# Optimization experiments

Measured on AMD Instinct MI355X. Metric: run time of the kernel, lower is better.

Reference implementation:

```python
import jax, jax.numpy as jnp
import numpy as np
import math

B, S, IN_DIM = 2048, 60, 211
D, H, L, DFF, NC = 192, 6, 3, 768, 35
DK = D // H


def make_pe(seq_len, d_model):
    pos = np.arange(seq_len)[:, None].astype(np.float32)
    div = np.exp(np.arange(0, d_model, 2).astype(np.float32) * (-math.log(10000.0) / d_model))
    pe = np.zeros((seq_len, d_model), dtype=np.float32)
    pe[:, 0::2] = np.sin(pos * div)
    pe[:, 1::2] = np.cos(pos * div)
    return jnp.asarray(pe)


def setup_inputs() -> dict:
    key = jax.random.key(0)
    ks = jax.random.split(key, 24)
    r = lambda k, shape, fan: jax.random.normal(k, shape, jnp.float32) * (1.0 / np.sqrt(fan))
    inp = {
        'x': jax.random.normal(ks[0], (B, S, IN_DIM), jnp.float32),
        'W_in': r(ks[1], (IN_DIM, D), IN_DIM), 'b_in': jnp.zeros((D,), jnp.float32),
        'pe': make_pe(S, D),
        'Wq': r(ks[2], (L, D, D), D), 'bq': jnp.zeros((L, D), jnp.float32),
        'Wk': r(ks[3], (L, D, D), D), 'bk': jnp.zeros((L, D), jnp.float32),
        'Wv': r(ks[4], (L, D, D), D), 'bv': jnp.zeros((L, D), jnp.float32),
        'Wo': r(ks[5], (L, D, D), D), 'bo': jnp.zeros((L, D), jnp.float32),
        'W1': r(ks[6], (L, D, DFF), D), 'b1': jnp.zeros((L, DFF), jnp.float32),
        'W2': r(ks[7], (L, DFF, D), DFF), 'b2': jnp.zeros((L, D), jnp.float32),
        'g1': jnp.ones((L, D), jnp.float32), 'be1': jnp.zeros((L, D), jnp.float32),
        'g2': jnp.ones((L, D), jnp.float32), 'be2': jnp.zeros((L, D), jnp.float32),
        'Wc1': r(ks[8], (D, D // 2), D), 'bc1': jnp.zeros((D // 2,), jnp.float32),
        'Wc2': r(ks[9], (D // 2, NC), D // 2), 'bc2': jnp.zeros((NC,), jnp.float32),
    }
    return inp


def layer_norm(x, g, b, eps=1e-5):
    mu = jnp.mean(x, axis=-1, keepdims=True)
    var = jnp.mean((x - mu) ** 2, axis=-1, keepdims=True)
    return (x - mu) * jax.lax.rsqrt(var + eps) * g + b


def mha(x, Wq, bq, Wk, bk, Wv, bv, Wo, bo):
    Bs, Ss, _ = x.shape
    q = (x @ Wq + bq).reshape(Bs, Ss, H, DK)
    k = (x @ Wk + bk).reshape(Bs, Ss, H, DK)
    v = (x @ Wv + bv).reshape(Bs, Ss, H, DK)
    scores = jnp.einsum('bqhd,bkhd->bhqk', q, k) / jnp.sqrt(jnp.float32(DK))
    attn = jax.nn.softmax(scores, axis=-1)
    ctx = jnp.einsum('bhqk,bkhd->bqhd', attn, v).reshape(Bs, Ss, D)
    return ctx @ Wo + bo


def encoder_layer(x, Wq, bq, Wk, bk, Wv, bv, Wo, bo, W1, b1, W2, b2, g1, be1, g2, be2):
    attn_out = mha(x, Wq, bq, Wk, bk, Wv, bv, Wo, bo)
    x = layer_norm(x + attn_out, g1, be1)
    ff = jax.nn.gelu(x @ W1 + b1, approximate=False) @ W2 + b2
    return layer_norm(x + ff, g2, be2)


def reference(x, W_in, b_in, pe, Wq, bq, Wk, bk, Wv, bv, Wo, bo,
              W1, b1, W2, b2, g1, be1, g2, be2, Wc1, bc1, Wc2, bc2):
    h = x @ W_in + b_in + pe  # [B,S,D]
    for l in range(L):
        h = encoder_layer(h, Wq[l], bq[l], Wk[l], bk[l], Wv[l], bv[l], Wo[l], bo[l],
                          W1[l], b1[l], W2[l], b2[l], g1[l], be1[l], g2[l], be2[l])
    hidden = jax.nn.gelu(h @ Wc1 + bc1, approximate=False)
    return hidden @ Wc2 + bc2  # [B,S,NC]
```

## Files before the change

### kernel.cpp

```cpp
#include <hip/hip_runtime.h>
#include <cmath>

#define B_   2048
#define S_   60
#define NTOK (B_*S_)
#define IND_ 211
#define D_   192
#define H_   6
#define DK_  32
#define L_   3
#define DFF_ 768
#define NC_  35
#define DH_  96

typedef unsigned short us_t;
typedef us_t us8 __attribute__((ext_vector_type(8)));
typedef us_t us4 __attribute__((ext_vector_type(4)));
typedef short sh8 __attribute__((ext_vector_type(8)));
typedef float f4 __attribute__((ext_vector_type(4)));

#define MFMA(a, b, cc) __builtin_amdgcn_mfma_f32_16x16x32_bf16((a), (b), (cc), 0, 0, 0)
#define ZACC(A, M, N) \
    for (int _i = 0; _i < (M); ++_i) \
        for (int _j = 0; _j < (N); ++_j) { \
            A[_i][_j][0] = 0.f; A[_i][_j][1] = 0.f; A[_i][_j][2] = 0.f; A[_i][_j][3] = 0.f; }
#define ZACC1(A, N) \
    for (int _j = 0; _j < (N); ++_j) { \
        A[_j][0] = 0.f; A[_j][1] = 0.f; A[_j][2] = 0.f; A[_j][3] = 0.f; }

__device__ __forceinline__ float bf2f(us_t u) {
    union { unsigned int i; float f; } v; v.i = ((unsigned int)u) << 16; return v.f;
}
__device__ __forceinline__ us_t f2bf(float f) {
    union { float f; unsigned int i; } v; v.f = f;
    unsigned int r = v.i + 0x7fffu + ((v.i >> 16) & 1u);
    return (us_t)(r >> 16);
}
__device__ __forceinline__ float gelu_f(float v) {
    float u = v * (0.7978845608f + 0.0356774081f * v * v);
    float e = __expf(2.f * u);
    float t = 1.f - 2.f / (e + 1.f);
    return 0.5f * v * (1.f + t);
}
__device__ __forceinline__ void gld16(const us_t* g, us_t* s) {
    __builtin_amdgcn_global_load_lds(
        (const __attribute__((address_space(1))) unsigned int*)(g),
        (__attribute__((address_space(3))) unsigned int*)(s), 16, 0, 0);
}

__global__ void prep_t(const float* __restrict__ in, us_t* __restrict__ out,
                       int K, int Kpad, int N)
{
    int e = blockIdx.x * 256 + threadIdx.x;
    if (e >= N * Kpad) return;
    int n = e / Kpad, kp = e % Kpad;
    out[e] = (kp < K) ? f2bf(in[(size_t)kp * N + n]) : (us_t)0;
}

__global__ void prep_ff(const float* __restrict__ W1, const float* __restrict__ W2,
                        us_t* __restrict__ W1T, us_t* __restrict__ W2T)
{
    int e = blockIdx.x * 256 + threadIdx.x;
    if (e >= L_ * 12 * 13824) return;
    int l = e / (12 * 13824), r = e % (12 * 13824);
    int tile = r / 13824, q = r % 13824;
    int col = q / 72, kk = q % 72;
    int cb = tile / 3, pc = tile % 3;
    us_t v1 = 0, v2 = 0;
    if (kk < 64) {
        v1 = f2bf(W1[((size_t)l * D_ + pc * 64 + kk) * DFF_ + cb * D_ + col]);
        v2 = f2bf(W2[((size_t)l * DFF_ + cb * D_ + pc * 64 + kk) * D_ + col]);
    }
    W1T[e] = v1; W2T[e] = v2;
}

__global__ __launch_bounds__(256) void inp_mfma(
    const float* __restrict__ x, const us_t* __restrict__ Wint,
    const float* __restrict__ b_in, const float* __restrict__ pe,
    us_t* __restrict__ h)
{
    __shared__ __align__(16) char smem[29696 + 27648];
    us_t* Xs = (us_t*)smem;
    us_t* Ws = (us_t*)(smem + 29696);
    const int tid = threadIdx.x;
    const int lane = tid & 63, wid = tid >> 6;
    const int g = lane >> 4, c = lane & 15;
    const int wr = wid >> 1, wc = wid & 1;
    const int row0 = blockIdx.x * 64;

    for (int e = tid; e < 64 * 224; e += 256) {
        int tok = e / 224, kp = e % 224;
        float v = (kp < IND_) ? x[(size_t)(row0 + tok) * IND_ + kp] : 0.f;
        Xs[tok * 232 + kp] = f2bf(v);
    }

    f4 acc[2][6];
    ZACC(acc, 2, 6);
    for (int pc = 0; pc < 4; ++pc) {
        __syncthreads();
        const int nk = (pc < 3) ? 64 : 32;
        const int per = nk / 8;
        for (int e = tid; e < 192 * per; e += 256) {
            int rw = e / per, v = e % per;
            *(us8*)&Ws[rw * 72 + v * 8] =
                *(const us8*)&Wint[(size_t)rw * 224 + pc * 64 + v * 8];
        }
        __syncthreads();
        for (int kk = 0; kk < nk / 32; ++kk) {
            const int ka = pc * 64 + kk * 32 + g * 8;
            const int kw = kk * 32 + g * 8;
            sh8 a0 = *(const sh8*)&Xs[(32 * wr + c) * 232 + ka];
            sh8 a1 = *(const sh8*)&Xs[(32 * wr + 16 + c) * 232 + ka];
            #pragma unroll
            for (int ni = 0; ni < 6; ++ni) {
                sh8 bf = *(const sh8*)&Ws[(96 * wc + 16 * ni + c) * 72 + kw];
                acc[0][ni] = MFMA(a0, bf, acc[0][ni]);
                acc[1][ni] = MFMA(a1, bf, acc[1][ni]);
            }
        }
    }
    #pragma unroll
    for (int ni = 0; ni < 6; ++ni) {
        const int col = 96 * wc + 16 * ni + c;
        const float bv = b_in[col];
        #pragma unroll
        for (int mi = 0; mi < 2; ++mi)
            #pragma unroll
            for (int r = 0; r < 4; ++r) {
                int tokg = row0 + 32 * wr + 16 * mi + 4 * g + r;
                int s = tokg % S_;
                float val = acc[mi][ni][r] + bv + pe[(size_t)s * D_ + col];
                h[(size_t)tokg * D_ + col] = f2bf(val);
            }
    }
}

__global__ __launch_bounds__(512) void qkv_attn_wo(
    us_t* __restrict__ h,
    const us_t* __restrict__ Wqt, const us_t* __restrict__ Wkt,
    const us_t* __restrict__ Wvt, const us_t* __restrict__ Wot,
    const float* __restrict__ bq, const float* __restrict__ bk,
    const float* __restrict__ bv, const float* __restrict__ bo,
    const float* __restrict__ g1, const float* __restrict__ be1)
{
    __shared__ __align__(16) char smem[157696];
    us_t* Xs = (us_t*)smem;
    us_t* Qs = (us_t*)(smem + 25600);
    us_t* Ks = (us_t*)(smem + 51200);
    us_t* Vt = (us_t*)(smem + 76800);
    us_t* Ws = (us_t*)(smem + 104448);
    us_t* P0 = (us_t*)(smem + 104448);
    us_t* P1 = (us_t*)(smem + 113664);
    us_t* Cx = (us_t*)(smem + 132096);
    float* eL = (float*)(smem + 51200);

    const int tid = threadIdx.x;
    const int lane = tid & 63, wid = tid >> 6;
    const int g = lane >> 4, c = lane & 15;
    const int wr = wid >> 2, wc = wid & 3;
    us_t* hb = h + (size_t)blockIdx.x * (S_ * D_);

    for (int e = tid; e < 1536; e += 512) {
        int tok = e / 24, v = e % 24;
        us8 u = {0, 0, 0, 0, 0, 0, 0, 0};
        if (tok < S_) u = *(const us8*)&hb[(size_t)tok * D_ + v * 8];
        *(us8*)&Xs[tok * 200 + v * 8] = u;
    }

    for (int m = 0; m < 3; ++m) {
        const us_t* Wt = (m == 0) ? Wqt : (m == 1) ? Wkt : Wvt;
        const float* bb = (m == 0) ? bq : (m == 1) ? bk : bv;
        f4 acc[2][3];
        ZACC(acc, 2, 3);
        for (int pc = 0; pc < 3; ++pc) {
            __syncthreads();
            for (int e = tid; e < 1536; e += 512) {
                int rw = e >> 3, v = e & 7;
                *(us8*)&Ws[rw * 72 + v * 8] =
                    *(const us8*)&Wt[(size_t)rw * 192 + pc * 64 + v * 8];
            }
            __syncthreads();
            #pragma unroll
            for (int kk = 0; kk < 2; ++kk) {
                const int ka = pc * 64 + kk * 32 + g * 8;
                const int kw = kk * 32 + g * 8;
                sh8 a0 = *(const sh8*)&Xs[(32 * wr + c) * 200 + ka];
                sh8 a1 = *(const sh8*)&Xs[(32 * wr + 16 + c) * 200 + ka];
                #pragma unroll
                for (int ni = 0; ni < 3; ++ni) {
                    sh8 bf = *(const sh8*)&Ws[(48 * wc + 16 * ni + c) * 72 + kw];
                    acc[0][ni] = MFMA(a0, bf, acc[0][ni]);
                    acc[1][ni] = MFMA(a1, bf, acc[1][ni]);
                }
            }
        }
        #pragma unroll
        for (int ni = 0; ni < 3; ++ni) {
            const int col = 48 * wc + 16 * ni + c;
            const float bval = bb[col];
            #pragma unroll
            for (int mi = 0; mi < 2; ++mi)
                #pragma unroll
                for (int r = 0; r < 4; ++r) {
                    int tok = 32 * wr + 16 * mi + 4 * g + r;
                    us_t o = f2bf(acc[mi][ni][r] + bval);
                    if (m == 0)      Qs[tok * 200 + col] = o;
                    else if (m == 1) Ks[tok * 200 + col] = o;
                    else             Vt[col * 72 + tok] = o;
                }
        }
    }
    __syncthreads();

    const int hgrp = wid & 3;
    const int hsel = wid >> 2;
    for (int rr = 0; rr < 3; ++rr) {
        const int hh = 2 * rr + hsel;
        us_t* Pb = hsel ? P1 : P0;
        f4 sc[4];
        ZACC1(sc, 4);
        {
            const int ka = 32 * hh + g * 8;
            sh8 aq = *(const sh8*)&Qs[(16 * hgrp + c) * 200 + ka];
            #pragma unroll
            for (int ni = 0; ni < 4; ++ni) {
                sh8 bk8 = *(const sh8*)&Ks[(16 * ni + c) * 200 + ka];
                sc[ni] = MFMA(aq, bk8, sc[ni]);
            }
        }
        #pragma unroll
        for (int r = 0; r < 4; ++r) {
            float mx = -1e30f;
            #pragma unroll
            for (int ni = 0; ni < 4; ++ni) {
                float v = sc[ni][r] * 0.17677669529663687f;
                if (16 * ni + c >= S_) v = -1e30f;
                sc[ni][r] = v;
                mx = fmaxf(mx, v);
            }
            mx = fmaxf(mx, __shfl_xor(mx, 1));
            mx = fmaxf(mx, __shfl_xor(mx, 2));
            mx = fmaxf(mx, __shfl_xor(mx, 4));
            mx = fmaxf(mx, __shfl_xor(mx, 8));
            float sum = 0.f;
            #pragma unroll
            for (int ni = 0; ni < 4; ++ni) {
                float e = __expf(sc[ni][r] - mx);
                sc[ni][r] = e; sum += e;
            }
            sum += __shfl_xor(sum, 1);
            sum += __shfl_xor(sum, 2);
            sum += __shfl_xor(sum, 4);
            sum += __shfl_xor(sum, 8);
            const float inv = 1.f / sum;
            #pragma unroll
            for (int ni = 0; ni < 4; ++ni)
                Pb[(16 * hgrp + 4 * g + r) * 72 + 16 * ni + c] = f2bf(sc[ni][r] * inv);
        }
        __syncthreads();
        f4 ov[2];
        ZACC1(ov, 2);
        #pragma unroll
        for (int kk = 0; kk < 2; ++kk) {
            sh8 ap = *(const sh8*)&Pb[(16 * hgrp + c) * 72 + kk * 32 + g * 8];
            #pragma unroll
            for (int n2 = 0; n2 < 2; ++n2) {
                sh8 bv8 = *(const sh8*)&Vt[(32 * hh + 16 * n2 + c) * 72 + kk * 32 + g * 8];
                ov[n2] = MFMA(ap, bv8, ov[n2]);
            }
        }
        #pragma unroll
        for (int n2 = 0; n2 < 2; ++n2)
            #pragma unroll
            for (int r = 0; r < 4; ++r)
                Cx[(16 * hgrp + 4 * g + r) * 200 + 32 * hh + 16 * n2 + c] = f2bf(ov[n2][r]);
        __syncthreads();
    }

    f4 aw[2][3];
    ZACC(aw, 2, 3);
    for (int pc = 0; pc < 3; ++pc) {
        __syncthreads();
        for (int e = tid; e < 1536; e += 512) {
            int rw = e >> 3, v = e & 7;
            *(us8*)&Ws[rw * 72 + v * 8] =
                *(const us8*)&Wot[(size_t)rw * 192 + pc * 64 + v * 8];
        }
        __syncthreads();
        #pragma unroll
        for (int kk = 0; kk < 2; ++kk) {
            const int ka = pc * 64 + kk * 32 + g * 8;
            const int kw = kk * 32 + g * 8;
            sh8 a0 = *(const sh8*)&Cx[(32 * wr + c) * 200 + ka];
            sh8 a1 = *(const sh8*)&Cx[(32 * wr + 16 + c) * 200 + ka];
            #pragma unroll
            for (int ni = 0; ni < 3; ++ni) {
                sh8 bf = *(const sh8*)&Ws[(48 * wc + 16 * ni + c) * 72 + kw];
                aw[0][ni] = MFMA(a0, bf, aw[0][ni]);
                aw[1][ni] = MFMA(a1, bf, aw[1][ni]);
            }
        }
    }
    __syncthreads();
    #pragma unroll
    for (int ni = 0; ni < 3; ++ni) {
        const int col = 48 * wc + 16 * ni + c;
        const float bov = bo[col];
        #pragma unroll
        for (int mi = 0; mi < 2; ++mi)
            #pragma unroll
            for (int r = 0; r < 4; ++r) {
                int tok = 32 * wr + 16 * mi + 4 * g + r;
                eL[tok * 200 + col] = aw[mi][ni][r] + bov + bf2f(Xs[tok * 200 + col]);
            }
    }
    __syncthreads();
    {
        const int tok = tid >> 3, t8 = tid & 7;
        float vals[24], sum = 0.f, ssq = 0.f;
        #pragma unroll
        for (int jv = 0; jv < 6; ++jv) {
            float4 v4 = *(const float4*)&eL[tok * 200 + t8 * 24 + jv * 4];
            vals[jv*4+0] = v4.x; vals[jv*4+1] = v4.y; vals[jv*4+2] = v4.z; vals[jv*4+3] = v4.w;
            sum += v4.x + v4.y + v4.z + v4.w;
            ssq += v4.x*v4.x + v4.y*v4.y + v4.z*v4.z + v4.w*v4.w;
        }
        sum += __shfl_xor(sum, 1); sum += __shfl_xor(sum, 2); sum += __shfl_xor(sum, 4);
        ssq += __shfl_xor(ssq, 1); ssq += __shfl_xor(ssq, 2); ssq += __shfl_xor(ssq, 4);
        const float mean = sum * (1.f / D_);
        const float var  = ssq * (1.f / D_) - mean * mean;
        const float rstd = rsqrtf(var + 1e-5f);
        if (tok < S_) {
            #pragma unroll
            for (int jv = 0; jv < 6; ++jv) {
                us4 o4;
                #pragma unroll
                for (int j = 0; j < 4; ++j) {
                    int col = t8 * 24 + jv * 4 + j;
                    o4[j] = f2bf((vals[jv*4+j] - mean) * rstd * g1[col] + be1[col]);
                }
                *(us4*)&hb[(size_t)tok * D_ + t8 * 24 + jv * 4] = o4;
            }
        }
    }
}

__device__ __forceinline__ void ff_tile(const us_t* A, f4 (&acc)[2][6],
                                        const us_t* W, int pc,
                                        int wr, int wc, int g, int c)
{
    #pragma unroll
    for (int kk = 0; kk < 2; ++kk) {
        const int ka = pc * 64 + kk * 32 + g * 8;
        const int kw = kk * 32 + g * 8;
        sh8 a0 = *(const sh8*)&A[(32 * wr + c) * 200 + ka];
        sh8 a1 = *(const sh8*)&A[(32 * wr + 16 + c) * 200 + ka];
        #pragma unroll
        for (int ni = 0; ni < 6; ++ni) {
            sh8 bf = *(const sh8*)&W[(96 * wc + 16 * ni + c) * 72 + kw];
            acc[0][ni] = MFMA(a0, bf, acc[0][ni]);
            acc[1][ni] = MFMA(a1, bf, acc[1][ni]);
        }
    }
}

__global__ __launch_bounds__(512) void ff_mfma(
    us_t* __restrict__ hio,
    const us_t* __restrict__ W1T, const float* __restrict__ b1,
    const us_t* __restrict__ W2T, const float* __restrict__ b2,
    const float* __restrict__ gamma, const float* __restrict__ beta)
{
    __shared__ __align__(16) char smem[157696];
    us_t* Xs  = (us_t*)smem;
    us_t* Ts  = (us_t*)(smem + 51200);
    us_t* Wsb = (us_t*)(smem + 102400);
    float* eL = (float*)(smem + 51200);

    const int tid = threadIdx.x;
    const int lane = tid & 63, wid = tid >> 6;
    const int g = lane >> 4, c = lane & 15;
    const int wr = wid >> 1, wc = wid & 1;
    const int row0 = blockIdx.x * 128;

    auto stageW = [&](int t) {
        const int cb2 = t / 6, ph = (t % 6) / 3, pc2 = t % 3;
        const us_t* src = (ph ? W2T : W1T) + (size_t)(cb2 * 3 + pc2) * 13824;
        us_t* dst = Wsb + (size_t)(t & 1) * 13824;
        #pragma unroll
        for (int i = wid; i < 27; i += 8)
            gld16(src + i * 512 + lane * 8, dst + i * 512);
    };

    for (int e = tid; e < 3072; e += 512) {
        int tok = e / 24, v = e % 24;
        *(us8*)&Xs[tok * 200 + v * 8] = *(const us8*)&hio[(size_t)(row0 + tok) * D_ + v * 8];
    }
    stageW(0);
    __syncthreads();

    f4 acc2[2][6];
    ZACC(acc2, 2, 6);
    for (int cb = 0; cb < 4; ++cb) {
        f4 acc1[2][6];
        ZACC(acc1, 2, 6);
        #pragma unroll
        for (int pc = 0; pc < 3; ++pc) {
            const int t = cb * 6 + pc;
            if (t < 23) stageW(t + 1);
            ff_tile(Xs, acc1, Wsb + (size_t)(t & 1) * 13824, pc, wr, wc, g, c);
            if (pc == 2) {
                #pragma unroll
                for (int ni = 0; ni < 6; ++ni) {
                    const int col = 96 * wc + 16 * ni + c;
                    const float b1v = b1[cb * 192 + col];
                    #pragma unroll
                    for (int mi = 0; mi < 2; ++mi)
                        #pragma unroll
                        for (int r = 0; r < 4; ++r) {
                            int tok = 32 * wr + 16 * mi + 4 * g + r;
                            Ts[tok * 200 + col] = f2bf(gelu_f(acc1[mi][ni][r] + b1v));
                        }
                }
            }
            __syncthreads();
        }
        #pragma unroll
        for (int pc = 0; pc < 3; ++pc) {
            const int t = cb * 6 + 3 + pc;
            if (t < 23) stageW(t + 1);
            ff_tile(Ts, acc2, Wsb + (size_t)(t & 1) * 13824, pc, wr, wc, g, c);
            __syncthreads();
        }
    }

    for (int p = 0; p < 2; ++p) {
        if (p) __syncthreads();
        if ((wr >> 1) == p) {
            #pragma unroll
            for (int ni = 0; ni < 6; ++ni) {
                const int col = 96 * wc + 16 * ni + c;
                const float b2v = b2[col];
                #pragma unroll
                for (int mi = 0; mi < 2; ++mi)
                    #pragma unroll
                    for (int r = 0; r < 4; ++r) {
                        int tok = 32 * wr + 16 * mi + 4 * g + r;
                        eL[(tok - 64 * p) * 200 + col] =
                            acc2[mi][ni][r] + b2v + bf2f(Xs[tok * 200 + col]);
                    }
            }
        }
        __syncthreads();
        {
            const int tl = tid >> 3, t8 = tid & 7;
            float vals[24], sum = 0.f, ssq = 0.f;
            #pragma unroll
            for (int jv = 0; jv < 6; ++jv) {
                float4 v4 = *(const float4*)&eL[tl * 200 + t8 * 24 + jv * 4];
                vals[jv*4+0] = v4.x; vals[jv*4+1] = v4.y;
                vals[jv*4+2] = v4.z; vals[jv*4+3] = v4.w;
                sum += v4.x + v4.y + v4.z + v4.w;
                ssq += v4.x*v4.x + v4.y*v4.y + v4.z*v4.z + v4.w*v4.w;
            }
            sum += __shfl_xor(sum, 1); sum += __shfl_xor(sum, 2); sum += __shfl_xor(sum, 4);
            ssq += __shfl_xor(ssq, 1); ssq += __shfl_xor(ssq, 2); ssq += __shfl_xor(ssq, 4);
            const float mean = sum * (1.f / D_);
            const float var  = ssq * (1.f / D_) - mean * mean;
            const float rstd = rsqrtf(var + 1e-5f);
            #pragma unroll
            for (int jv = 0; jv < 6; ++jv) {
                us4 o4;
                #pragma unroll
                for (int j = 0; j < 4; ++j) {
                    int col = t8 * 24 + jv * 4 + j;
                    o4[j] = f2bf((vals[jv*4+j] - mean) * rstd * gamma[col] + beta[col]);
                }
                *(us4*)&hio[(size_t)(row0 + 64 * p + tl) * D_ + t8 * 24 + jv * 4] = o4;
            }
        }
    }
}

__global__ __launch_bounds__(256) void clf1_mfma(
    const us_t* __restrict__ h, const us_t* __restrict__ Wc1t,
    const float* __restrict__ bc1, us_t* __restrict__ hid)
{
    __shared__ __align__(16) char smem[25600 + 13824];
    us_t* Xs = (us_t*)smem;
    us_t* Ws = (us_t*)(smem + 25600);
    const int tid = threadIdx.x;
    const int lane = tid & 63, wid = tid >> 6;
    const int g = lane >> 4, c = lane & 15;
    const int wr = wid >> 1, wc = wid & 1;
    const int row0 = blockIdx.x * 64;

    for (int e = tid; e < 1536; e += 256) {
        int tok = e / 24, v = e % 24;
        *(us8*)&Xs[tok * 200 + v * 8] = *(const us8*)&h[(size_t)(row0 + tok) * D_ + v * 8];
    }
    f4 acc[2][3];
    ZACC(acc, 2, 3);
    for (int pc = 0; pc < 3; ++pc) {
        __syncthreads();
        for (int e = tid; e < 768; e += 256) {
            int rw = e >> 3, v = e & 7;
            *(us8*)&Ws[rw * 72 + v * 8] =
                *(const us8*)&Wc1t[(size_t)rw * 192 + pc * 64 + v * 8];
        }
        __syncthreads();
        #pragma unroll
        for (int kk = 0; kk < 2; ++kk) {
            const int ka = pc * 64 + kk * 32 + g * 8;
            const int kw = kk * 32 + g * 8;
            sh8 a0 = *(const sh8*)&Xs[(32 * wr + c) * 200 + ka];
            sh8 a1 = *(const sh8*)&Xs[(32 * wr + 16 + c) * 200 + ka];
            #pragma unroll
            for (int ni = 0; ni < 3; ++ni) {
                sh8 bf = *(const sh8*)&Ws[(48 * wc + 16 * ni + c) * 72 + kw];
                acc[0][ni] = MFMA(a0, bf, acc[0][ni]);
                acc[1][ni] = MFMA(a1, bf, acc[1][ni]);
            }
        }
    }
    #pragma unroll
    for (int ni = 0; ni < 3; ++ni) {
        const int col = 48 * wc + 16 * ni + c;
        const float bv = bc1[col];
        #pragma unroll
        for (int mi = 0; mi < 2; ++mi)
            #pragma unroll
            for (int r = 0; r < 4; ++r) {
                int tok = row0 + 32 * wr + 16 * mi + 4 * g + r;
                hid[(size_t)tok * DH_ + col] = f2bf(gelu_f(acc[mi][ni][r] + bv));
            }
    }
}

__global__ __launch_bounds__(256) void clf2_kernel(
    const us_t* __restrict__ hid, const float* __restrict__ Wc2,
    const float* __restrict__ bc2, float* __restrict__ out)
{
    __shared__ us_t Hs[64 * 104];
    __shared__ float Wl[DH_ * NC_];
    __shared__ float bl[NC_];
    const int tid = threadIdx.x;
    const int row0 = blockIdx.x * 64;
    for (int e = tid; e < 768; e += 256) {
        int tok = e / 12, v = e % 12;
        *(us8*)&Hs[tok * 104 + v * 8] = *(const us8*)&hid[(size_t)(row0 + tok) * DH_ + v * 8];
    }
    for (int e = tid; e < DH_ * NC_; e += 256) Wl[e] = Wc2[e];
    if (tid < NC_) bl[tid] = bc2[tid];
    __syncthreads();
    for (int e = tid; e < 64 * NC_; e += 256) {
        const int tok = e / NC_, col = e % NC_;
        float acc = bl[col];
        #pragma unroll 8
        for (int kk = 0; kk < DH_; ++kk)
            acc = fmaf(bf2f(Hs[tok * 104 + kk]), Wl[kk * NC_ + col], acc);
        out[(size_t)(row0 + tok) * NC_ + col] = acc;
    }
}

extern "C" void kernel_launch(void* const* d_in, const int* in_sizes, int n_in,
                              void* d_out, int out_size, void* d_ws, size_t ws_size,
                              hipStream_t stream)
{
    const float* x    = (const float*)d_in[0];
    const float* W_in = (const float*)d_in[1];
    const float* b_in = (const float*)d_in[2];
    const float* pe   = (const float*)d_in[3];
    const float* Wq   = (const float*)d_in[4];
    const float* bq   = (const float*)d_in[5];
    const float* Wk   = (const float*)d_in[6];
    const float* bk   = (const float*)d_in[7];
    const float* Wv   = (const float*)d_in[8];
    const float* bv   = (const float*)d_in[9];
    const float* Wo   = (const float*)d_in[10];
    const float* bo   = (const float*)d_in[11];
    const float* W1   = (const float*)d_in[12];
    const float* b1   = (const float*)d_in[13];
    const float* W2   = (const float*)d_in[14];
    const float* b2   = (const float*)d_in[15];
    const float* g1   = (const float*)d_in[16];
    const float* be1  = (const float*)d_in[17];
    const float* g2   = (const float*)d_in[18];
    const float* be2  = (const float*)d_in[19];
    const float* Wc1  = (const float*)d_in[20];
    const float* bc1  = (const float*)d_in[21];
    const float* Wc2  = (const float*)d_in[22];
    const float* bc2  = (const float*)d_in[23];
    float* outp = (float*)d_out;

    us_t* h    = (us_t*)d_ws;
    us_t* hid  = h + (size_t)NTOK * D_;
    us_t* Wint = hid + (size_t)NTOK * DH_;
    us_t* Wqt  = Wint + 192 * 224;
    us_t* Wkt  = Wqt + 3 * 36864;
    us_t* Wvt  = Wkt + 3 * 36864;
    us_t* Wot  = Wvt + 3 * 36864;
    us_t* W1T  = Wot + 3 * 36864;
    us_t* W2T  = W1T + (size_t)L_ * 12 * 13824;
    us_t* Wc1t = W2T + (size_t)L_ * 12 * 13824;

    prep_t<<<168, 256, 0, stream>>>(W_in, Wint, IND_, 224, D_);
    for (int l = 0; l < L_; ++l) {
        prep_t<<<144, 256, 0, stream>>>(Wq + (size_t)l * 36864, Wqt + (size_t)l * 36864, 192, 192, 192);
        prep_t<<<144, 256, 0, stream>>>(Wk + (size_t)l * 36864, Wkt + (size_t)l * 36864, 192, 192, 192);
        prep_t<<<144, 256, 0, stream>>>(Wv + (size_t)l * 36864, Wvt + (size_t)l * 36864, 192, 192, 192);
        prep_t<<<144, 256, 0, stream>>>(Wo + (size_t)l * 36864, Wot + (size_t)l * 36864, 192, 192, 192);
    }
    prep_ff<<<(L_ * 12 * 13824 + 255) / 256, 256, 0, stream>>>(W1, W2, W1T, W2T);
    prep_t<<<72, 256, 0, stream>>>(Wc1, Wc1t, 192, 192, DH_);

    inp_mfma<<<NTOK / 64, 256, 0, stream>>>(x, Wint, b_in, pe, h);

    for (int l = 0; l < L_; ++l) {
        qkv_attn_wo<<<B_, 512, 0, stream>>>(
            h,
            Wqt + (size_t)l * 36864, Wkt + (size_t)l * 36864,
            Wvt + (size_t)l * 36864, Wot + (size_t)l * 36864,
            bq + l * D_, bk + l * D_, bv + l * D_, bo + l * D_,
            g1 + l * D_, be1 + l * D_);
        ff_mfma<<<NTOK / 128, 512, 0, stream>>>(
            h, W1T + (size_t)l * 12 * 13824, b1 + l * DFF_,
            W2T + (size_t)l * 12 * 13824, b2 + l * D_,
            g2 + l * D_, be2 + l * D_);
    }

    clf1_mfma<<<NTOK / 64, 256, 0, stream>>>(h, Wc1t, bc1, hid);
    clf2_kernel<<<NTOK / 64, 256, 0, stream>>>(hid, Wc2, bc2, outp);
}
```

Measured before the change: 1.233 ms.

## Triple-buffer FF weight tiles with finer K-slices and vmcnt-based barriers

Restructures the FFN kernel's weight streaming into 48 smaller K=32 tiles in one interleaved buffer, staged two tiles ahead into a 3-slot LDS ring. The old __syncthreads is replaced by s_waitcnt vmcnt(2) plus a raw barrier, so loads stay in flight across iterations. This aims to hide global-to-LDS latency behind MFMA work and cut wait time at each barrier. In exchange it adds twice as many barriers, since the tiles are half as deep, and it depends on hand-written waitcnt counts being correct.

```diff
diff --git a/kernel.cpp b/kernel.cpp
--- a/kernel.cpp
+++ b/kernel.cpp
@@ -58,20 +58,20 @@
 }
 
 __global__ void prep_ff(const float* __restrict__ W1, const float* __restrict__ W2,
-                        us_t* __restrict__ W1T, us_t* __restrict__ W2T)
+                        us_t* __restrict__ WT)
 {
     int e = blockIdx.x * 256 + threadIdx.x;
-    if (e >= L_ * 12 * 13824) return;
-    int l = e / (12 * 13824), r = e % (12 * 13824);
-    int tile = r / 13824, q = r % 13824;
-    int col = q / 72, kk = q % 72;
-    int cb = tile / 3, pc = tile % 3;
-    us_t v1 = 0, v2 = 0;
-    if (kk < 64) {
-        v1 = f2bf(W1[((size_t)l * D_ + pc * 64 + kk) * DFF_ + cb * D_ + col]);
-        v2 = f2bf(W2[((size_t)l * DFF_ + cb * D_ + pc * 64 + kk) * D_ + col]);
-    }
-    W1T[e] = v1; W2T[e] = v2;
+    if (e >= L_ * 48 * 8192) return;
+    int l = e / (48 * 8192), r = e % (48 * 8192);
+    int t = r / 8192, q = r % 8192;
+    int col = q / 40, kk = q % 40;
+    int s = t % 6, ph = (t / 6) & 1, cb = t / 12;
+    us_t v = 0;
+    if (kk < 32 && col < D_) {
+        if (!ph) v = f2bf(W1[((size_t)l * D_ + s * 32 + kk) * DFF_ + cb * D_ + col]);
+        else     v = f2bf(W2[((size_t)l * DFF_ + cb * D_ + s * 32 + kk) * D_ + col]);
+    }
+    WT[e] = v;
 }
 
 __global__ __launch_bounds__(256) void inp_mfma(
@@ -345,32 +345,28 @@
     }
 }
 
-__device__ __forceinline__ void ff_tile(const us_t* A, f4 (&acc)[2][6],
-                                        const us_t* W, int pc,
-                                        int wr, int wc, int g, int c)
-{
+__device__ __forceinline__ void ff_phase(const us_t* A, f4 (&acc)[2][6],
+                                         const us_t* W, int s,
+                                         int wr, int wc, int g, int c)
+{
+    const int ka = s * 32 + g * 8;
+    sh8 a0 = *(const sh8*)&A[(32 * wr + c) * 200 + ka];
+    sh8 a1 = *(const sh8*)&A[(32 * wr + 16 + c) * 200 + ka];
     #pragma unroll
-    for (int kk = 0; kk < 2; ++kk) {
-        const int ka = pc * 64 + kk * 32 + g * 8;
-        const int kw = kk * 32 + g * 8;
-        sh8 a0 = *(const sh8*)&A[(32 * wr + c) * 200 + ka];
-        sh8 a1 = *(const sh8*)&A[(32 * wr + 16 + c) * 200 + ka];
-        #pragma unroll
-        for (int ni = 0; ni < 6; ++ni) {
-            sh8 bf = *(const sh8*)&W[(96 * wc + 16 * ni + c) * 72 + kw];
-            acc[0][ni] = MFMA(a0, bf, acc[0][ni]);
-            acc[1][ni] = MFMA(a1, bf, acc[1][ni]);
-        }
+    for (int ni = 0; ni < 6; ++ni) {
+        sh8 bf = *(const sh8*)&W[(96 * wc + 16 * ni + c) * 40 + g * 8];
+        acc[0][ni] = MFMA(a0, bf, acc[0][ni]);
+        acc[1][ni] = MFMA(a1, bf, acc[1][ni]);
     }
 }
 
 __global__ __launch_bounds__(512) void ff_mfma(
     us_t* __restrict__ hio,
-    const us_t* __restrict__ W1T, const float* __restrict__ b1,
-    const us_t* __restrict__ W2T, const float* __restrict__ b2,
+    const us_t* __restrict__ WT, const float* __restrict__ b1,
+    const float* __restrict__ b2,
     const float* __restrict__ gamma, const float* __restrict__ beta)
 {
-    __shared__ __align__(16) char smem[157696];
+    __shared__ __align__(16) char smem[151552];
     us_t* Xs  = (us_t*)smem;
     us_t* Ts  = (us_t*)(smem + 51200);
     us_t* Wsb = (us_t*)(smem + 102400);
@@ -382,33 +378,35 @@
     const int wr = wid >> 1, wc = wid & 1;
     const int row0 = blockIdx.x * 128;
 
-    auto stageW = [&](int t) {
-        const int cb2 = t / 6, ph = (t % 6) / 3, pc2 = t % 3;
-        const us_t* src = (ph ? W2T : W1T) + (size_t)(cb2 * 3 + pc2) * 13824;
-        us_t* dst = Wsb + (size_t)(t & 1) * 13824;
-        #pragma unroll
-        for (int i = wid; i < 27; i += 8)
+    auto stage = [&](int t) {
+        const us_t* src = WT + (size_t)t * 8192;
+        us_t* dst = Wsb + (t % 3) * 8192;
+        #pragma unroll
+        for (int p = 0; p < 2; ++p) {
+            const int i = wid + p * 8;
             gld16(src + i * 512 + lane * 8, dst + i * 512);
+        }
     };
 
     for (int e = tid; e < 3072; e += 512) {
         int tok = e / 24, v = e % 24;
         *(us8*)&Xs[tok * 200 + v * 8] = *(const us8*)&hio[(size_t)(row0 + tok) * D_ + v * 8];
     }
-    stageW(0);
-    __syncthreads();
-
-    f4 acc2[2][6];
+    stage(0); stage(1);
+    asm volatile("s_waitcnt vmcnt(2) lgkmcnt(0)" ::: "memory");
+    __builtin_amdgcn_s_barrier();
+
+    f4 acc1[2][6], acc2[2][6];
     ZACC(acc2, 2, 6);
-    for (int cb = 0; cb < 4; ++cb) {
-        f4 acc1[2][6];
-        ZACC(acc1, 2, 6);
-        #pragma unroll
-        for (int pc = 0; pc < 3; ++pc) {
-            const int t = cb * 6 + pc;
-            if (t < 23) stageW(t + 1);
-            ff_tile(Xs, acc1, Wsb + (size_t)(t & 1) * 13824, pc, wr, wc, g, c);
-            if (pc == 2) {
+    for (int t = 0; t < 48; ++t) {
+        const int s = t % 6, ph = (t / 6) & 1;
+        if (t <= 45) stage(t + 2);
+        const us_t* W = Wsb + (t % 3) * 8192;
+        if (!ph) {
+            if (s == 0) ZACC(acc1, 2, 6);
+            ff_phase(Xs, acc1, W, s, wr, wc, g, c);
+            if (s == 5) {
+                const int cb = t / 12;
                 #pragma unroll
                 for (int ni = 0; ni < 6; ++ni) {
                     const int col = 96 * wc + 16 * ni + c;
@@ -422,15 +420,12 @@
                         }
                 }
             }
-            __syncthreads();
-        }
-        #pragma unroll
-        for (int pc = 0; pc < 3; ++pc) {
-            const int t = cb * 6 + 3 + pc;
-            if (t < 23) stageW(t + 1);
-            ff_tile(Ts, acc2, Wsb + (size_t)(t & 1) * 13824, pc, wr, wc, g, c);
-            __syncthreads();
-        }
+        } else {
+            ff_phase(Ts, acc2, W, s, wr, wc, g, c);
+        }
+        if (t <= 45) asm volatile("s_waitcnt vmcnt(2) lgkmcnt(0)" ::: "memory");
+        else         asm volatile("s_waitcnt vmcnt(0) lgkmcnt(0)" ::: "memory");
+        __builtin_amdgcn_s_barrier();
     }
 
     for (int p = 0; p < 2; ++p) {
@@ -599,9 +594,8 @@
     us_t* Wkt  = Wqt + 3 * 36864;
     us_t* Wvt  = Wkt + 3 * 36864;
     us_t* Wot  = Wvt + 3 * 36864;
-    us_t* W1T  = Wot + 3 * 36864;
-    us_t* W2T  = W1T + (size_t)L_ * 12 * 13824;
-    us_t* Wc1t = W2T + (size_t)L_ * 12 * 13824;
+    us_t* WT   = Wot + 3 * 36864;
+    us_t* Wc1t = WT + (size_t)L_ * 48 * 8192;
 
     prep_t<<<168, 256, 0, stream>>>(W_in, Wint, IND_, 224, D_);
     for (int l = 0; l < L_; ++l) {
@@ -610,7 +604,7 @@
         prep_t<<<144, 256, 0, stream>>>(Wv + (size_t)l * 36864, Wvt + (size_t)l * 36864, 192, 192, 192);
         prep_t<<<144, 256, 0, stream>>>(Wo + (size_t)l * 36864, Wot + (size_t)l * 36864, 192, 192, 192);
     }
-    prep_ff<<<(L_ * 12 * 13824 + 255) / 256, 256, 0, stream>>>(W1, W2, W1T, W2T);
+    prep_ff<<<(L_ * 48 * 8192 + 255) / 256, 256, 0, stream>>>(W1, W2, WT);
     prep_t<<<72, 256, 0, stream>>>(Wc1, Wc1t, 192, 192, DH_);
 
     inp_mfma<<<NTOK / 64, 256, 0, stream>>>(x, Wint, b_in, pe, h);
@@ -623,8 +617,7 @@
             bq + l * D_, bk + l * D_, bv + l * D_, bo + l * D_,
             g1 + l * D_, be1 + l * D_);
         ff_mfma<<<NTOK / 128, 512, 0, stream>>>(
-            h, W1T + (size_t)l * 12 * 13824, b1 + l * DFF_,
-            W2T + (size_t)l * 12 * 13824, b2 + l * D_,
+            h, WT + (size_t)l * 48 * 8192, b1 + l * DFF_, b2 + l * D_,
             g2 + l * D_, be2 + l * D_);
     }
 
```

Measured after the change: 1.342 ms. 1.09x slower.

## Double threads per block in attention and FFN kernels to 1024

Applied to the files above, without the earlier changes.

Both the fused attention block kernel and the FFN kernel now launch 16 waves instead of 8, and each wave computes a smaller output tile (fewer accumulators per wave). Attention heads are spread over 12 active waves in two rounds instead of 8 waves in three rounds, and the LayerNorm epilogues use 16 threads per token. The goal is more latency hiding and lower register pressure per wave, since LDS usage (~154KB) already limits each CU to one block. In exchange, weight fragments are reloaded from LDS more often per MFMA, and some waves sit idle during attention.

```diff
diff --git a/kernel.cpp b/kernel.cpp
--- a/kernel.cpp
+++ b/kernel.cpp
@@ -135,7 +135,7 @@
     }
 }
 
-__global__ __launch_bounds__(512) void qkv_attn_wo(
+__global__ __launch_bounds__(1024) void qkv_attn_wo(
     us_t* __restrict__ h,
     const us_t* __restrict__ Wqt, const us_t* __restrict__ Wkt,
     const us_t* __restrict__ Wvt, const us_t* __restrict__ Wot,
@@ -144,14 +144,13 @@
     const float* __restrict__ g1, const float* __restrict__ be1)
 {
     __shared__ __align__(16) char smem[157696];
-    us_t* Xs = (us_t*)smem;
-    us_t* Qs = (us_t*)(smem + 25600);
-    us_t* Ks = (us_t*)(smem + 51200);
-    us_t* Vt = (us_t*)(smem + 76800);
-    us_t* Ws = (us_t*)(smem + 104448);
-    us_t* P0 = (us_t*)(smem + 104448);
-    us_t* P1 = (us_t*)(smem + 113664);
-    us_t* Cx = (us_t*)(smem + 132096);
+    us_t* Xs  = (us_t*)smem;
+    us_t* Qs  = (us_t*)(smem + 25600);
+    us_t* Ks  = (us_t*)(smem + 51200);
+    us_t* Vt  = (us_t*)(smem + 76800);
+    us_t* Ws  = (us_t*)(smem + 104448);
+    us_t* Pb3 = (us_t*)(smem + 104448);
+    us_t* Cx  = (us_t*)(smem + 132096);
     float* eL = (float*)(smem + 51200);
 
     const int tid = threadIdx.x;
@@ -160,7 +159,7 @@
     const int wr = wid >> 2, wc = wid & 3;
     us_t* hb = h + (size_t)blockIdx.x * (S_ * D_);
 
-    for (int e = tid; e < 1536; e += 512) {
+    for (int e = tid; e < 1536; e += 1024) {
         int tok = e / 24, v = e % 24;
         us8 u = {0, 0, 0, 0, 0, 0, 0, 0};
         if (tok < S_) u = *(const us8*)&hb[(size_t)tok * D_ + v * 8];
@@ -170,16 +169,220 @@
     for (int m = 0; m < 3; ++m) {
         const us_t* Wt = (m == 0) ? Wqt : (m == 1) ? Wkt : Wvt;
         const float* bb = (m == 0) ? bq : (m == 1) ? bk : bv;
-        f4 acc[2][3];
-        ZACC(acc, 2, 3);
+        f4 acc[3];
+        ZACC1(acc, 3);
         for (int pc = 0; pc < 3; ++pc) {
             __syncthreads();
-            for (int e = tid; e < 1536; e += 512) {
+            for (int e = tid; e < 1536; e += 1024) {
                 int rw = e >> 3, v = e & 7;
                 *(us8*)&Ws[rw * 72 + v * 8] =
                     *(const us8*)&Wt[(size_t)rw * 192 + pc * 64 + v * 8];
             }
             __syncthreads();
+            #pragma unroll
+            for (int kk = 0; kk < 2; ++kk) {
+                const int ka = pc * 64 + kk * 32 + g * 8;
+                const int kw = kk * 32 + g * 8;
+                sh8 a0 = *(const sh8*)&Xs[(16 * wr + c) * 200 + ka];
+                #pragma unroll
+                for (int ni = 0; ni < 3; ++ni) {
+                    sh8 bf = *(const sh8*)&Ws[(48 * wc + 16 * ni + c) * 72 + kw];
+                    acc[ni] = MFMA(a0, bf, acc[ni]);
+                }
+            }
+        }
+        #pragma unroll
+        for (int ni = 0; ni < 3; ++ni) {
+            const int col = 48 * wc + 16 * ni + c;
+            const float bval = bb[col];
+            #pragma unroll
+            for (int r = 0; r < 4; ++r) {
+                int tok = 16 * wr + 4 * g + r;
+                us_t o = f2bf(acc[ni][r] + bval);
+                if (m == 0)      Qs[tok * 200 + col] = o;
+                else if (m == 1) Ks[tok * 200 + col] = o;
+                else             Vt[col * 72 + tok] = o;
+            }
+        }
+    }
+    __syncthreads();
+
+    for (int rr2 = 0; rr2 < 2; ++rr2) {
+        const bool act = (wid < 12);
+        const int hh = 3 * rr2 + (wid >> 2);
+        const int hgrp = wid & 3;
+        us_t* Pb = Pb3 + (size_t)(wid >> 2) * 4608;
+        if (act) {
+            f4 sc[4];
+            ZACC1(sc, 4);
+            const int ka = 32 * hh + g * 8;
+            sh8 aq = *(const sh8*)&Qs[(16 * hgrp + c) * 200 + ka];
+            #pragma unroll
+            for (int ni = 0; ni < 4; ++ni) {
+                sh8 bk8 = *(const sh8*)&Ks[(16 * ni + c) * 200 + ka];
+                sc[ni] = MFMA(aq, bk8, sc[ni]);
+            }
+            #pragma unroll
+            for (int r = 0; r < 4; ++r) {
+                float mx = -1e30f;
+                #pragma unroll
+                for (int ni = 0; ni < 4; ++ni) {
+                    float v = sc[ni][r] * 0.17677669529663687f;
+                    if (16 * ni + c >= S_) v = -1e30f;
+                    sc[ni][r] = v;
+                    mx = fmaxf(mx, v);
+                }
+                mx = fmaxf(mx, __shfl_xor(mx, 1));
+                mx = fmaxf(mx, __shfl_xor(mx, 2));
+                mx = fmaxf(mx, __shfl_xor(mx, 4));
+                mx = fmaxf(mx, __shfl_xor(mx, 8));
+                float sum = 0.f;
+                #pragma unroll
+                for (int ni = 0; ni < 4; ++ni) {
+                    float e = __expf(sc[ni][r] - mx);
+                    sc[ni][r] = e; sum += e;
+                }
+                sum += __shfl_xor(sum, 1);
+                sum += __shfl_xor(sum, 2);
+                sum += __shfl_xor(sum, 4);
+                sum += __shfl_xor(sum, 8);
+                const float inv = 1.f / sum;
+                #pragma unroll
+                for (int ni = 0; ni < 4; ++ni)
+                    Pb[(16 * hgrp + 4 * g + r) * 72 + 16 * ni + c] = f2bf(sc[ni][r] * inv);
+            }
+        }
+        __syncthreads();
+        if (act) {
+            f4 ov[2];
+            ZACC1(ov, 2);
+            #pragma unroll
+            for (int kk = 0; kk < 2; ++kk) {
+                sh8 ap = *(const sh8*)&Pb[(16 * hgrp + c) * 72 + kk * 32 + g * 8];
+                #pragma unroll
+                for (int n2 = 0; n2 < 2; ++n2) {
+                    sh8 bv8 = *(const sh8*)&Vt[(32 * hh + 16 * n2 + c) * 72 + kk * 32 + g * 8];
+                    ov[n2] = MFMA(ap, bv8, ov[n2]);
+                }
+            }
+            #pragma unroll
+            for (int n2 = 0; n2 < 2; ++n2)
+                #pragma unroll
+                for (int r = 0; r < 4; ++r)
+                    Cx[(16 * hgrp + 4 * g + r) * 200 + 32 * hh + 16 * n2 + c] = f2bf(ov[n2][r]);
+        }
+        __syncthreads();
+    }
+
+    f4 aw[3];
+    ZACC1(aw, 3);
+    for (int pc = 0; pc < 3; ++pc) {
+        __syncthreads();
+        for (int e = tid; e < 1536; e += 1024) {
+            int rw = e >> 3, v = e & 7;
+            *(us8*)&Ws[rw * 72 + v * 8] =
+                *(const us8*)&Wot[(size_t)rw * 192 + pc * 64 + v * 8];
+        }
+        __syncthreads();
+        #pragma unroll
+        for (int kk = 0; kk < 2; ++kk) {
+            const int ka = pc * 64 + kk * 32 + g * 8;
+            const int kw = kk * 32 + g * 8;
+            sh8 a0 = *(const sh8*)&Cx[(16 * wr + c) * 200 + ka];
+            #pragma unroll
+            for (int ni = 0; ni < 3; ++ni) {
+                sh8 bf = *(const sh8*)&Ws[(48 * wc + 16 * ni + c) * 72 + kw];
+                aw[ni] = MFMA(a0, bf, aw[ni]);
+            }
+        }
+    }
+    __syncthreads();
+    #pragma unroll
+    for (int ni = 0; ni < 3; ++ni) {
+        const int col = 48 * wc + 16 * ni + c;
+        const float bov = bo[col];
+        #pragma unroll
+        for (int r = 0; r < 4; ++r) {
+            int tok = 16 * wr + 4 * g + r;
+            eL[tok * 200 + col] = aw[ni][r] + bov + bf2f(Xs[tok * 200 + col]);
+        }
+    }
+    __syncthreads();
+    {
+        const int tl = tid >> 4, t16 = tid & 15;
+        float vals[12], sum = 0.f, ssq = 0.f;
+        #pragma unroll
+        for (int jv = 0; jv < 3; ++jv) {
+            float4 v4 = *(const float4*)&eL[tl * 200 + t16 * 12 + jv * 4];
+            vals[jv*4+0] = v4.x; vals[jv*4+1] = v4.y; vals[jv*4+2] = v4.z; vals[jv*4+3] = v4.w;
+            sum += v4.x + v4.y + v4.z + v4.w;
+            ssq += v4.x*v4.x + v4.y*v4.y + v4.z*v4.z + v4.w*v4.w;
+        }
+        sum += __shfl_xor(sum, 1); sum += __shfl_xor(sum, 2);
+        sum += __shfl_xor(sum, 4); sum += __shfl_xor(sum, 8);
+        ssq += __shfl_xor(ssq, 1); ssq += __shfl_xor(ssq, 2);
+        ssq += __shfl_xor(ssq, 4); ssq += __shfl_xor(ssq, 8);
+        const float mean = sum * (1.f / D_);
+        const float var  = ssq * (1.f / D_) - mean * mean;
+        const float rstd = rsqrtf(var + 1e-5f);
+        if (tl < S_) {
+            #pragma unroll
+            for (int jv = 0; jv < 3; ++jv) {
+                us4 o4;
+                #pragma unroll
+                for (int j = 0; j < 4; ++j) {
+                    int col = t16 * 12 + jv * 4 + j;
+                    o4[j] = f2bf((vals[jv*4+j] - mean) * rstd * g1[col] + be1[col]);
+                }
+                *(us4*)&hb[(size_t)tl * D_ + t16 * 12 + jv * 4] = o4;
+            }
+        }
+    }
+}
+
+__global__ __launch_bounds__(1024) void ff_mfma(
+    us_t* __restrict__ hio,
+    const us_t* __restrict__ W1T, const float* __restrict__ b1,
+    const us_t* __restrict__ W2T, const float* __restrict__ b2,
+    const float* __restrict__ gamma, const float* __restrict__ beta)
+{
+    __shared__ __align__(16) char smem[157696];
+    us_t* Xs  = (us_t*)smem;
+    us_t* Ts  = (us_t*)(smem + 51200);
+    us_t* Wsb = (us_t*)(smem + 102400);
+    float* eL = (float*)(smem + 51200);
+
+    const int tid = threadIdx.x;
+    const int lane = tid & 63, wid = tid >> 6;
+    const int g = lane >> 4, c = lane & 15;
+    const int wr = wid >> 2, wc = wid & 3;
+    const int row0 = blockIdx.x * 128;
+
+    auto stageW = [&](int t) {
+        const int cb2 = t / 6, ph = (t % 6) / 3, pc2 = t % 3;
+        const us_t* src = (ph ? W2T : W1T) + (size_t)(cb2 * 3 + pc2) * 13824;
+        us_t* dst = Wsb + (size_t)(t & 1) * 13824;
+        for (int i = wid; i < 27; i += 16)
+            gld16(src + i * 512 + lane * 8, dst + i * 512);
+    };
+
+    for (int e = tid; e < 3072; e += 1024) {
+        int tok = e / 24, v = e % 24;
+        *(us8*)&Xs[tok * 200 + v * 8] = *(const us8*)&hio[(size_t)(row0 + tok) * D_ + v * 8];
+    }
+    stageW(0);
+    __syncthreads();
+
+    f4 acc2[2][3];
+    ZACC(acc2, 2, 3);
+    for (int cb = 0; cb < 4; ++cb) {
+        f4 acc1[2][3];
+        ZACC(acc1, 2, 3);
+        #pragma unroll
+        for (int pc = 0; pc < 3; ++pc) {
+            const int t = cb * 6 + pc;
+            if (t < 23) stageW(t + 1);
+            const us_t* W = Wsb + (size_t)(t & 1) * 13824;
             #pragma unroll
             for (int kk = 0; kk < 2; ++kk) {
                 const int ka = pc * 64 + kk * 32 + g * 8;
@@ -188,230 +391,15 @@
                 sh8 a1 = *(const sh8*)&Xs[(32 * wr + 16 + c) * 200 + ka];
                 #pragma unroll
                 for (int ni = 0; ni < 3; ++ni) {
-                    sh8 bf = *(const sh8*)&Ws[(48 * wc + 16 * ni + c) * 72 + kw];
-                    acc[0][ni] = MFMA(a0, bf, acc[0][ni]);
-                    acc[1][ni] = MFMA(a1, bf, acc[1][ni]);
-                }
-            }
-        }
-        #pragma unroll
-        for (int ni = 0; ni < 3; ++ni) {
-            const int col = 48 * wc + 16 * ni + c;
-            const float bval = bb[col];
-            #pragma unroll
-            for (int mi = 0; mi < 2; ++mi)
-                #pragma unroll
-                for (int r = 0; r < 4; ++r) {
-                    int tok = 32 * wr + 16 * mi + 4 * g + r;
-                    us_t o = f2bf(acc[mi][ni][r] + bval);
-                    if (m == 0)      Qs[tok * 200 + col] = o;
-                    else if (m == 1) Ks[tok * 200 + col] = o;
-                    else             Vt[col * 72 + tok] = o;
-                }
-        }
-    }
-    __syncthreads();
-
-    const int hgrp = wid & 3;
-    const int hsel = wid >> 2;
-    for (int rr = 0; rr < 3; ++rr) {
-        const int hh = 2 * rr + hsel;
-        us_t* Pb = hsel ? P1 : P0;
-        f4 sc[4];
-        ZACC1(sc, 4);
-        {
-            const int ka = 32 * hh + g * 8;
-            sh8 aq = *(const sh8*)&Qs[(16 * hgrp + c) * 200 + ka];
-            #pragma unroll
-            for (int ni = 0; ni < 4; ++ni) {
-                sh8 bk8 = *(const sh8*)&Ks[(16 * ni + c) * 200 + ka];
-                sc[ni] = MFMA(aq, bk8, sc[ni]);
-            }
-        }
-        #pragma unroll
-        for (int r = 0; r < 4; ++r) {
-            float mx = -1e30f;
-            #pragma unroll
-            for (int ni = 0; ni < 4; ++ni) {
-                float v = sc[ni][r] * 0.17677669529663687f;
-                if (16 * ni + c >= S_) v = -1e30f;
-                sc[ni][r] = v;
-                mx = fmaxf(mx, v);
-            }
-            mx = fmaxf(mx, __shfl_xor(mx, 1));
-            mx = fmaxf(mx, __shfl_xor(mx, 2));
-            mx = fmaxf(mx, __shfl_xor(mx, 4));
-            mx = fmaxf(mx, __shfl_xor(mx, 8));
-            float sum = 0.f;
-            #pragma unroll
-            for (int ni = 0; ni < 4; ++ni) {
-                float e = __expf(sc[ni][r] - mx);
-                sc[ni][r] = e; sum += e;
-            }
-            sum += __shfl_xor(sum, 1);
-            sum += __shfl_xor(sum, 2);
-            sum += __shfl_xor(sum, 4);
-            sum += __shfl_xor(sum, 8);
-            const float inv = 1.f / sum;
-            #pragma unroll
-            for (int ni = 0; ni < 4; ++ni)
-                Pb[(16 * hgrp + 4 * g + r) * 72 + 16 * ni + c] = f2bf(sc[ni][r] * inv);
-        }
-        __syncthreads();
-        f4 ov[2];
-        ZACC1(ov, 2);
-        #pragma unroll
-        for (int kk = 0; kk < 2; ++kk) {
-            sh8 ap = *(const sh8*)&Pb[(16 * hgrp + c) * 72 + kk * 32 + g * 8];
-            #pragma unroll
-            for (int n2 = 0; n2 < 2; ++n2) {
-                sh8 bv8 = *(const sh8*)&Vt[(32 * hh + 16 * n2 + c) * 72 + kk * 32 + g * 8];
-                ov[n2] = MFMA(ap, bv8, ov[n2]);
-            }
-        }
-        #pragma unroll
-        for (int n2 = 0; n2 < 2; ++n2)
-            #pragma unroll
-            for (int r = 0; r < 4; ++r)
-                Cx[(16 * hgrp + 4 * g + r) * 200 + 32 * hh + 16 * n2 + c] = f2bf(ov[n2][r]);
-        __syncthreads();
-    }
-
-    f4 aw[2][3];
-    ZACC(aw, 2, 3);
-    for (int pc = 0; pc < 3; ++pc) {
-        __syncthreads();
-        for (int e = tid; e < 1536; e += 512) {
-            int rw = e >> 3, v = e & 7;
-            *(us8*)&Ws[rw * 72 + v * 8] =
-                *(const us8*)&Wot[(size_t)rw * 192 + pc * 64 + v * 8];
-        }
-        __syncthreads();
-        #pragma unroll
-        for (int kk = 0; kk < 2; ++kk) {
-            const int ka = pc * 64 + kk * 32 + g * 8;
-            const int kw = kk * 32 + g * 8;
-            sh8 a0 = *(const sh8*)&Cx[(32 * wr + c) * 200 + ka];
-            sh8 a1 = *(const sh8*)&Cx[(32 * wr + 16 + c) * 200 + ka];
-            #pragma unroll
-            for (int ni = 0; ni < 3; ++ni) {
-                sh8 bf = *(const sh8*)&Ws[(48 * wc + 16 * ni + c) * 72 + kw];
-                aw[0][ni] = MFMA(a0, bf, aw[0][ni]);
-                aw[1][ni] = MFMA(a1, bf, aw[1][ni]);
-            }
-        }
-    }
-    __syncthreads();
-    #pragma unroll
-    for (int ni = 0; ni < 3; ++ni) {
-        const int col = 48 * wc + 16 * ni + c;
-        const float bov = bo[col];
-        #pragma unroll
-        for (int mi = 0; mi < 2; ++mi)
-            #pragma unroll
-            for (int r = 0; r < 4; ++r) {
-                int tok = 32 * wr + 16 * mi + 4 * g + r;
-                eL[tok * 200 + col] = aw[mi][ni][r] + bov + bf2f(Xs[tok * 200 + col]);
-            }
-    }
-    __syncthreads();
-    {
-        const int tok = tid >> 3, t8 = tid & 7;
-        float vals[24], sum = 0.f, ssq = 0.f;
-        #pragma unroll
-        for (int jv = 0; jv < 6; ++jv) {
-            float4 v4 = *(const float4*)&eL[tok * 200 + t8 * 24 + jv * 4];
-            vals[jv*4+0] = v4.x; vals[jv*4+1] = v4.y; vals[jv*4+2] = v4.z; vals[jv*4+3] = v4.w;
-            sum += v4.x + v4.y + v4.z + v4.w;
-            ssq += v4.x*v4.x + v4.y*v4.y + v4.z*v4.z + v4.w*v4.w;
-        }
-        sum += __shfl_xor(sum, 1); sum += __shfl_xor(sum, 2); sum += __shfl_xor(sum, 4);
-        ssq += __shfl_xor(ssq, 1); ssq += __shfl_xor(ssq, 2); ssq += __shfl_xor(ssq, 4);
-        const float mean = sum * (1.f / D_);
-        const float var  = ssq * (1.f / D_) - mean * mean;
-        const float rstd = rsqrtf(var + 1e-5f);
-        if (tok < S_) {
-            #pragma unroll
-            for (int jv = 0; jv < 6; ++jv) {
-                us4 o4;
-                #pragma unroll
-                for (int j = 0; j < 4; ++j) {
-                    int col = t8 * 24 + jv * 4 + j;
-                    o4[j] = f2bf((vals[jv*4+j] - mean) * rstd * g1[col] + be1[col]);
-                }
-                *(us4*)&hb[(size_t)tok * D_ + t8 * 24 + jv * 4] = o4;
-            }
-        }
-    }
-}
-
-__device__ __forceinline__ void ff_tile(const us_t* A, f4 (&acc)[2][6],
-                                        const us_t* W, int pc,
-                                        int wr, int wc, int g, int c)
-{
-    #pragma unroll
-    for (int kk = 0; kk < 2; ++kk) {
-        const int ka = pc * 64 + kk * 32 + g * 8;
-        const int kw = kk * 32 + g * 8;
-        sh8 a0 = *(const sh8*)&A[(32 * wr + c) * 200 + ka];
-        sh8 a1 = *(const sh8*)&A[(32 * wr + 16 + c) * 200 + ka];
-        #pragma unroll
-        for (int ni = 0; ni < 6; ++ni) {
-            sh8 bf = *(const sh8*)&W[(96 * wc + 16 * ni + c) * 72 + kw];
-            acc[0][ni] = MFMA(a0, bf, acc[0][ni]);
-            acc[1][ni] = MFMA(a1, bf, acc[1][ni]);
-        }
-    }
-}
-
-__global__ __launch_bounds__(512) void ff_mfma(
-    us_t* __restrict__ hio,
-    const us_t* __restrict__ W1T, const float* __restrict__ b1,
-    const us_t* __restrict__ W2T, const float* __restrict__ b2,
-    const float* __restrict__ gamma, const float* __restrict__ beta)
-{
-    __shared__ __align__(16) char smem[157696];
-    us_t* Xs  = (us_t*)smem;
-    us_t* Ts  = (us_t*)(smem + 51200);
-    us_t* Wsb = (us_t*)(smem + 102400);
-    float* eL = (float*)(smem + 51200);
-
-    const int tid = threadIdx.x;
-    const int lane = tid & 63, wid = tid >> 6;
-    const int g = lane >> 4, c = lane & 15;
-    const int wr = wid >> 1, wc = wid & 1;
-    const int row0 = blockIdx.x * 128;
-
-    auto stageW = [&](int t) {
-        const int cb2 = t / 6, ph = (t % 6) / 3, pc2 = t % 3;
-        const us_t* src = (ph ? W2T : W1T) + (size_t)(cb2 * 3 + pc2) * 13824;
-        us_t* dst = Wsb + (size_t)(t & 1) * 13824;
-        #pragma unroll
-        for (int i = wid; i < 27; i += 8)
-            gld16(src + i * 512 + lane * 8, dst + i * 512);
-    };
-
-    for (int e = tid; e < 3072; e += 512) {
-        int tok = e / 24, v = e % 24;
-        *(us8*)&Xs[tok * 200 + v * 8] = *(const us8*)&hio[(size_t)(row0 + tok) * D_ + v * 8];
-    }
-    stageW(0);
-    __syncthreads();
-
-    f4 acc2[2][6];
-    ZACC(acc2, 2, 6);
-    for (int cb = 0; cb < 4; ++cb) {
-        f4 acc1[2][6];
-        ZACC(acc1, 2, 6);
-        #pragma unroll
-        for (int pc = 0; pc < 3; ++pc) {
-            const int t = cb * 6 + pc;
-            if (t < 23) stageW(t + 1);
-            ff_tile(Xs, acc1, Wsb + (size_t)(t & 1) * 13824, pc, wr, wc, g, c);
+                    sh8 bf = *(const sh8*)&W[(48 * wc + 16 * ni + c) * 72 + kw];
+                    acc1[0][ni] = MFMA(a0, bf, acc1[0][ni]);
+                    acc1[1][ni] = MFMA(a1, bf, acc1[1][ni]);
+                }
+            }
             if (pc == 2) {
                 #pragma unroll
-                for (int ni = 0; ni < 6; ++ni) {
-                    const int col = 96 * wc + 16 * ni + c;
+                for (int ni = 0; ni < 3; ++ni) {
+                    const int col = 48 * wc + 16 * ni + c;
                     const float b1v = b1[cb * 192 + col];
                     #pragma unroll
                     for (int mi = 0; mi < 2; ++mi)
@@ -428,7 +416,20 @@
         for (int pc = 0; pc < 3; ++pc) {
             const int t = cb * 6 + 3 + pc;
             if (t < 23) stageW(t + 1);
-            ff_tile(Ts, acc2, Wsb + (size_t)(t & 1) * 13824, pc, wr, wc, g, c);
+            const us_t* W = Wsb + (size_t)(t & 1) * 13824;
+            #pragma unroll
+            for (int kk = 0; kk < 2; ++kk) {
+                const int ka = pc * 64 + kk * 32 + g * 8;
+                const int kw = kk * 32 + g * 8;
+                sh8 a0 = *(const sh8*)&Ts[(32 * wr + c) * 200 + ka];
+                sh8 a1 = *(const sh8*)&Ts[(32 * wr + 16 + c) * 200 + ka];
+                #pragma unroll
+                for (int ni = 0; ni < 3; ++ni) {
+                    sh8 bf = *(const sh8*)&W[(48 * wc + 16 * ni + c) * 72 + kw];
+                    acc2[0][ni] = MFMA(a0, bf, acc2[0][ni]);
+                    acc2[1][ni] = MFMA(a1, bf, acc2[1][ni]);
+                }
+            }
             __syncthreads();
         }
     }
@@ -437,8 +438,8 @@
         if (p) __syncthreads();
         if ((wr >> 1) == p) {
             #pragma unroll
-            for (int ni = 0; ni < 6; ++ni) {
-                const int col = 96 * wc + 16 * ni + c;
+            for (int ni = 0; ni < 3; ++ni) {
+                const int col = 48 * wc + 16 * ni + c;
                 const float b2v = b2[col];
                 #pragma unroll
                 for (int mi = 0; mi < 2; ++mi)
@@ -452,30 +453,32 @@
         }
         __syncthreads();
         {
-            const int tl = tid >> 3, t8 = tid & 7;
-            float vals[24], sum = 0.f, ssq = 0.f;
-            #pragma unroll
-            for (int jv = 0; jv < 6; ++jv) {
-                float4 v4 = *(const float4*)&eL[tl * 200 + t8 * 24 + jv * 4];
+            const int tl = tid >> 4, t16 = tid & 15;
+            float vals[12], sum = 0.f, ssq = 0.f;
+            #pragma unroll
+            for (int jv = 0; jv < 3; ++jv) {
+                float4 v4 = *(const float4*)&eL[tl * 200 + t16 * 12 + jv * 4];
                 vals[jv*4+0] = v4.x; vals[jv*4+1] = v4.y;
                 vals[jv*4+2] = v4.z; vals[jv*4+3] = v4.w;
                 sum += v4.x + v4.y + v4.z + v4.w;
                 ssq += v4.x*v4.x + v4.y*v4.y + v4.z*v4.z + v4.w*v4.w;
             }
-            sum += __shfl_xor(sum, 1); sum += __shfl_xor(sum, 2); sum += __shfl_xor(sum, 4);
-            ssq += __shfl_xor(ssq, 1); ssq += __shfl_xor(ssq, 2); ssq += __shfl_xor(ssq, 4);
+            sum += __shfl_xor(sum, 1); sum += __shfl_xor(sum, 2);
+            sum += __shfl_xor(sum, 4); sum += __shfl_xor(sum, 8);
+            ssq += __shfl_xor(ssq, 1); ssq += __shfl_xor(ssq, 2);
+            ssq += __shfl_xor(ssq, 4); ssq += __shfl_xor(ssq, 8);
             const float mean = sum * (1.f / D_);
             const float var  = ssq * (1.f / D_) - mean * mean;
             const float rstd = rsqrtf(var + 1e-5f);
             #pragma unroll
-            for (int jv = 0; jv < 6; ++jv) {
+            for (int jv = 0; jv < 3; ++jv) {
                 us4 o4;
                 #pragma unroll
                 for (int j = 0; j < 4; ++j) {
-                    int col = t8 * 24 + jv * 4 + j;
+                    int col = t16 * 12 + jv * 4 + j;
                     o4[j] = f2bf((vals[jv*4+j] - mean) * rstd * gamma[col] + beta[col]);
                 }
-                *(us4*)&hio[(size_t)(row0 + 64 * p + tl) * D_ + t8 * 24 + jv * 4] = o4;
+                *(us4*)&hio[(size_t)(row0 + 64 * p + tl) * D_ + t16 * 12 + jv * 4] = o4;
             }
         }
     }
@@ -616,13 +619,13 @@
     inp_mfma<<<NTOK / 64, 256, 0, stream>>>(x, Wint, b_in, pe, h);
 
     for (int l = 0; l < L_; ++l) {
-        qkv_attn_wo<<<B_, 512, 0, stream>>>(
+        qkv_attn_wo<<<B_, 1024, 0, stream>>>(
             h,
             Wqt + (size_t)l * 36864, Wkt + (size_t)l * 36864,
             Wvt + (size_t)l * 36864, Wot + (size_t)l * 36864,
             bq + l * D_, bk + l * D_, bv + l * D_, bo + l * D_,
             g1 + l * D_, be1 + l * D_);
-        ff_mfma<<<NTOK / 128, 512, 0, stream>>>(
+        ff_mfma<<<NTOK / 128, 1024, 0, stream>>>(
             h, W1T + (size_t)l * 12 * 13824, b1 + l * DFF_,
             W2T + (size_t)l * 12 * 13824, b2 + l * D_,
             g2 + l * D_, be2 + l * D_);
```

Result: faster. 1.180 ms (-4.3%).
